# Kernel optimization log

Hardware: AMD Instinct MI355X
Metric: run time of the kernel (lower is better)

Reference implementation:

```python
import jax, jax.numpy as jnp
import numpy as np

B, S, D = 32, 2048, 64

def setup_inputs() -> dict:
    key = jax.random.key(0)
    kq, kk, kv = jax.random.split(key, 3)
    return {
        "query": jax.random.normal(kq, (B, S, D), dtype=jnp.float32),
        "key": jax.random.normal(kk, (B, S, D), dtype=jnp.float32),
        "value": jax.random.normal(kv, (B, S, D), dtype=jnp.float32),
    }

def reference(query, key, value):
    # scores: [B, S, S] = Q @ K^T / sqrt(d_k)  (scale=True)
    d_k = key.shape[-1]
    scores = jnp.einsum("bqd,bkd->bqk", query, key) / jnp.sqrt(jnp.asarray(d_k, query.dtype))
    # exp + normalize over last dim == softmax (no mask, dropout in eval mode)
    attn = jax.nn.softmax(scores, axis=-1)
    # context: [B, S, D] = attn @ V
    context = jnp.einsum("bqk,bkd->bqd", attn, value)
    return context
```

## Files before the change

kernel.cpp:

```cpp
#include <hip/hip_runtime.h>
#include <hip/hip_bf16.h>

#define B_   32
#define S_   2048
#define D_   64
#define KVB  64
#define NT   (S_/KVB)
#define NW   8
#define QW   32
#define QB   (NW*QW)

typedef __attribute__((ext_vector_type(8)))  __bf16 bf16x8;
typedef __attribute__((ext_vector_type(4)))  __bf16 bf16x4;
typedef __attribute__((ext_vector_type(16))) float  f32x16;

__device__ __forceinline__ float fexp2(float x) {
#if __has_builtin(__builtin_amdgcn_exp2f)
    return __builtin_amdgcn_exp2f(x);
#else
    return exp2f(x);
#endif
}

__device__ __forceinline__ unsigned pk2(float a, float b) {
    unsigned r;
    asm("v_cvt_pk_bf16_f32 %0, %1, %2" : "=v"(r) : "v"(a), "v"(b));
    return r;
}

__device__ __forceinline__ void pl32swap(unsigned &a, unsigned &b) {
#if __has_builtin(__builtin_amdgcn_permlane32_swap)
    auto r = __builtin_amdgcn_permlane32_swap(a, b, false, false);
    a = (unsigned)r[0]; b = (unsigned)r[1];
#else
    unsigned pa = (unsigned)__shfl_xor((int)a, 32);
    unsigned pb = (unsigned)__shfl_xor((int)b, 32);
    bool hi = (threadIdx.x & 32) != 0;
    unsigned na = hi ? pb : a;
    unsigned nb = hi ? b  : pa;
    a = na; b = nb;
#endif
}

__device__ __forceinline__ f32x16 z16() {
    f32x16 z;
    #pragma unroll
    for (int i = 0; i < 16; ++i) z[i] = 0.f;
    return z;
}

struct PBpair { bf16x8 a, b; };

__device__ __forceinline__ PBpair pack2(const f32x16 ps) {
    unsigned y0 = pk2(ps[0],  ps[1]);
    unsigned y1 = pk2(ps[2],  ps[3]);
    unsigned y2 = pk2(ps[4],  ps[5]);
    unsigned y3 = pk2(ps[6],  ps[7]);
    pl32swap(y0, y2); pl32swap(y1, y3);
    unsigned z0 = pk2(ps[8],  ps[9]);
    unsigned z1 = pk2(ps[10], ps[11]);
    unsigned z2 = pk2(ps[12], ps[13]);
    unsigned z3 = pk2(ps[14], ps[15]);
    pl32swap(z0, z2); pl32swap(z1, z3);
    union { unsigned u[4]; bf16x8 v; } pa, pbu;
    pa.u[0]=y0;  pa.u[1]=y1;  pa.u[2]=y2;  pa.u[3]=y3;
    pbu.u[0]=z0; pbu.u[1]=z1; pbu.u[2]=z2; pbu.u[3]=z3;
    PBpair r; r.a = pa.v; r.b = pbu.v; return r;
}

__global__ __launch_bounds__(512, 2)
void attn_fwd(const float* __restrict__ Q, const float* __restrict__ K,
              const float* __restrict__ V, float* __restrict__ Out)
{
    __shared__ __align__(16) __bf16 Kt[2][KVB * D_];
    __shared__ __align__(16) __bf16 Vt[2][D_ * KVB];

    const int tid  = threadIdx.x;
    const int w    = tid >> 6;
    const int lane = tid & 63;
    const int l31  = lane & 31;
    const int hi   = lane >> 5;

    const int bid = blockIdx.x;
    const int swz = ((bid & 7) << 5) | (bid >> 3);
    const int b   = swz >> 3;
    const int q0  = (swz & 7) * QB;

    const float SCL = 0.18033688011112042f;
    const float* qp = Q + ((size_t)(b*S_ + q0 + w*QW + l31))*D_ + hi*8;
    bf16x8 qf[4];
    #pragma unroll
    for (int ks = 0; ks < 4; ++ks) {
        float4 f0 = *reinterpret_cast<const float4*>(qp + ks*16);
        float4 f1 = *reinterpret_cast<const float4*>(qp + ks*16 + 4);
        bf16x8 a;
        a[0]=(__bf16)(f0.x*SCL); a[1]=(__bf16)(f0.y*SCL);
        a[2]=(__bf16)(f0.z*SCL); a[3]=(__bf16)(f0.w*SCL);
        a[4]=(__bf16)(f1.x*SCL); a[5]=(__bf16)(f1.y*SCL);
        a[6]=(__bf16)(f1.z*SCL); a[7]=(__bf16)(f1.w*SCL);
        qf[ks]=a;
    }

    const int swzk = (l31 & 7) << 4;
    int offK[4];
    #pragma unroll
    for (int i = 0; i < 4; ++i)
        offK[i] = l31*128 + (((i*32) + hi*16) ^ swzk);

    const float* kg = K + (size_t)b*S_*D_;
    const float* vg = V + (size_t)b*S_*D_;

    const int krow0 = tid >> 4;
    const int kcol  = (tid & 15) * 4;
    const int kwr0  = krow0*128 + ((kcol*2) ^ ((krow0 & 7) << 4));
    const int kwr1  = kwr0 + 32*128;

    const int kv0 = (tid >> 4) * 2;
    const int db  = (tid & 15) * 2;
    int vwr[4];
    #pragma unroll
    for (int j = 0; j < 4; ++j) {
        int d = db + (j >> 1)*32 + (j & 1);
        vwr[j] = d*128 + ((kv0*2) ^ ((d & 7) << 4));
    }

    {
        float4 ka  = *reinterpret_cast<const float4*>(kg + krow0*64 + kcol);
        float4 kb  = *reinterpret_cast<const float4*>(kg + (krow0+32)*64 + kcol);
        float2 va0 = *reinterpret_cast<const float2*>(vg + kv0*64 + db);
        float2 vb0 = *reinterpret_cast<const float2*>(vg + (kv0+1)*64 + db);
        float2 va1 = *reinterpret_cast<const float2*>(vg + kv0*64 + db + 32);
        float2 vb1 = *reinterpret_cast<const float2*>(vg + (kv0+1)*64 + db + 32);
        char* kw = (char*)&Kt[0][0];
        char* vw = (char*)&Vt[0][0];
        bf16x4 h0 = {(__bf16)ka.x,(__bf16)ka.y,(__bf16)ka.z,(__bf16)ka.w};
        bf16x4 h1 = {(__bf16)kb.x,(__bf16)kb.y,(__bf16)kb.z,(__bf16)kb.w};
        *reinterpret_cast<bf16x4*>(kw + kwr0) = h0;
        *reinterpret_cast<bf16x4*>(kw + kwr1) = h1;
        *reinterpret_cast<unsigned*>(vw + vwr[0]) = pk2(va0.x, vb0.x);
        *reinterpret_cast<unsigned*>(vw + vwr[1]) = pk2(va0.y, vb0.y);
        *reinterpret_cast<unsigned*>(vw + vwr[2]) = pk2(va1.x, vb1.x);
        *reinterpret_cast<unsigned*>(vw + vwr[3]) = pk2(va1.y, vb1.y);
    }
    __syncthreads();

    float m_ = -INFINITY, l_ = 0.f;
    f32x16 o0 = z16(), o1 = z16();

    #pragma unroll 2
    for (int t = 0; t < NT; ++t) {
        const int cur = t & 1;

        const int tn = (t+1 < NT) ? (t+1) : t;
        const float* kt_ = kg + tn*KVB*D_;
        const float* vt_ = vg + tn*KVB*D_;
        float4 ka  = *reinterpret_cast<const float4*>(kt_ + krow0*64 + kcol);
        float4 kb  = *reinterpret_cast<const float4*>(kt_ + (krow0+32)*64 + kcol);
        float2 va0 = *reinterpret_cast<const float2*>(vt_ + kv0*64 + db);
        float2 vb0 = *reinterpret_cast<const float2*>(vt_ + (kv0+1)*64 + db);
        float2 va1 = *reinterpret_cast<const float2*>(vt_ + kv0*64 + db + 32);
        float2 vb1 = *reinterpret_cast<const float2*>(vt_ + (kv0+1)*64 + db + 32);

        const char* kbuf = (const char*)&Kt[cur][0];
        const char* vbuf = (const char*)&Vt[cur][0];

        f32x16 s0 = z16(), s1 = z16();
        __builtin_amdgcn_s_setprio(1);
        #pragma unroll
        for (int ks = 0; ks < 4; ++ks) {
            bf16x8 k0 = *reinterpret_cast<const bf16x8*>(kbuf + offK[ks]);
            bf16x8 k1 = *reinterpret_cast<const bf16x8*>(kbuf + offK[ks] + 4096);
            s0 = __builtin_amdgcn_mfma_f32_32x32x16_bf16(k0, qf[ks], s0, 0,0,0);
            s1 = __builtin_amdgcn_mfma_f32_32x32x16_bf16(k1, qf[ks], s1, 0,0,0);
        }
        __builtin_amdgcn_s_setprio(0);

        float pmax = s0[0];
        #pragma unroll
        for (int r = 1; r < 16; ++r) pmax = fmaxf(pmax, s0[r]);
        #pragma unroll
        for (int r = 0; r < 16; ++r) pmax = fmaxf(pmax, s1[r]);
        pmax = fmaxf(pmax, __shfl_xor(pmax, 32));
        if (!__all(pmax - m_ <= 8.0f)) {
            float mn  = fmaxf(m_, pmax);
            float fac = fexp2(m_ - mn);
            m_ = mn; l_ *= fac;
            #pragma unroll
            for (int r = 0; r < 16; ++r) { o0[r] *= fac; o1[r] *= fac; }
        }
        float lsum = 0.f;
        #pragma unroll
        for (int r = 0; r < 16; ++r) { s0[r] = fexp2(s0[r] - m_); lsum += s0[r]; }
        #pragma unroll
        for (int r = 0; r < 16; ++r) { s1[r] = fexp2(s1[r] - m_); lsum += s1[r]; }
        lsum += __shfl_xor(lsum, 32);
        l_ += lsum;

        PBpair p01 = pack2(s0);
        PBpair p23 = pack2(s1);

        __builtin_amdgcn_s_setprio(1);
        #define PV_STEP(c, pbf)                                                        \
        {   bf16x8 v0 = *reinterpret_cast<const bf16x8*>(vbuf + offK[c]);              \
            bf16x8 v1 = *reinterpret_cast<const bf16x8*>(vbuf + offK[c] + 4096);       \
            o0 = __builtin_amdgcn_mfma_f32_32x32x16_bf16(v0, pbf, o0, 0,0,0);          \
            o1 = __builtin_amdgcn_mfma_f32_32x32x16_bf16(v1, pbf, o1, 0,0,0);          }
        PV_STEP(0, p01.a)
        PV_STEP(1, p01.b)
        PV_STEP(2, p23.a)
        PV_STEP(3, p23.b)
        #undef PV_STEP
        __builtin_amdgcn_s_setprio(0);

        if (t+1 < NT) {
            char* kw = (char*)&Kt[cur^1][0];
            char* vw = (char*)&Vt[cur^1][0];
            bf16x4 h0 = {(__bf16)ka.x,(__bf16)ka.y,(__bf16)ka.z,(__bf16)ka.w};
            bf16x4 h1 = {(__bf16)kb.x,(__bf16)kb.y,(__bf16)kb.z,(__bf16)kb.w};
            *reinterpret_cast<bf16x4*>(kw + kwr0) = h0;
            *reinterpret_cast<bf16x4*>(kw + kwr1) = h1;
            *reinterpret_cast<unsigned*>(vw + vwr[0]) = pk2(va0.x, vb0.x);
            *reinterpret_cast<unsigned*>(vw + vwr[1]) = pk2(va0.y, vb0.y);
            *reinterpret_cast<unsigned*>(vw + vwr[2]) = pk2(va1.x, vb1.x);
            *reinterpret_cast<unsigned*>(vw + vwr[3]) = pk2(va1.y, vb1.y);
        }
        __syncthreads();
    }

    float invl = 1.0f / l_;
    float* orow = Out + ((size_t)(b*S_ + q0 + w*QW + l31))*D_;
    #pragma unroll
    for (int rr = 0; rr < 4; ++rr) {
        float4 res;
        res.x = o0[rr*4+0]*invl; res.y = o0[rr*4+1]*invl;
        res.z = o0[rr*4+2]*invl; res.w = o0[rr*4+3]*invl;
        *reinterpret_cast<float4*>(orow + rr*8 + hi*4) = res;
    }
    #pragma unroll
    for (int rr = 0; rr < 4; ++rr) {
        float4 res;
        res.x = o1[rr*4+0]*invl; res.y = o1[rr*4+1]*invl;
        res.z = o1[rr*4+2]*invl; res.w = o1[rr*4+3]*invl;
        *reinterpret_cast<float4*>(orow + 32 + rr*8 + hi*4) = res;
    }
}

extern "C" void kernel_launch(void* const* d_in, const int* in_sizes, int n_in,
                              void* d_out, int out_size, void* d_ws, size_t ws_size,
                              hipStream_t stream) {
    const float* Q = (const float*)d_in[0];
    const float* K = (const float*)d_in[1];
    const float* V = (const float*)d_in[2];
    float* O = (float*)d_out;
    attn_fwd<<<dim3(B_ * (S_ / QB)), dim3(512), 0, stream>>>(Q, K, V, O);
}
```

Before: 56.49 us.

## Halve workgroup to four waves and turn softmax reductions into trees

Cuts each workgroup from 8 to 4 waves (128 query rows), so the grid doubles to 512 blocks. The block swizzle is updated, and each thread now stages twice as many K/V elements per tile into LDS. The row max and row sum are also rewritten as pairwise tree reductions to shorten the serial dependency chains. The aim is better load balance across CUs and more latency hiding, at the cost of each K/V tile being loaded and converted by twice as many blocks and more registers per thread.

After: 66.34 us. +17.4%, slower.

```diff
diff --git a/kernel.cpp b/kernel.cpp
--- a/kernel.cpp
+++ b/kernel.cpp
@@ -6,7 +6,7 @@
 #define D_   64
 #define KVB  64
 #define NT   (S_/KVB)
-#define NW   8
+#define NW   4
 #define QW   32
 #define QB   (NW*QW)
 
@@ -68,7 +68,7 @@
     PBpair r; r.a = pa.v; r.b = pbu.v; return r;
 }
 
-__global__ __launch_bounds__(512, 2)
+__global__ __launch_bounds__(256, 2)
 void attn_fwd(const float* __restrict__ Q, const float* __restrict__ K,
               const float* __restrict__ V, float* __restrict__ Out)
 {
@@ -82,9 +82,9 @@
     const int hi   = lane >> 5;
 
     const int bid = blockIdx.x;
-    const int swz = ((bid & 7) << 5) | (bid >> 3);
-    const int b   = swz >> 3;
-    const int q0  = (swz & 7) * QB;
+    const int swz = ((bid & 7) << 6) | (bid >> 3);
+    const int b   = swz >> 4;
+    const int q0  = (swz & 15) * QB;
 
     const float SCL = 0.18033688011112042f;
     const float* qp = Q + ((size_t)(b*S_ + q0 + w*QW + l31))*D_ + hi*8;
@@ -113,34 +113,34 @@
     const int krow0 = tid >> 4;
     const int kcol  = (tid & 15) * 4;
     const int kwr0  = krow0*128 + ((kcol*2) ^ ((krow0 & 7) << 4));
-    const int kwr1  = kwr0 + 32*128;
 
     const int kv0 = (tid >> 4) * 2;
     const int db  = (tid & 15) * 2;
-    int vwr[4];
-    #pragma unroll
-    for (int j = 0; j < 4; ++j) {
-        int d = db + (j >> 1)*32 + (j & 1);
-        vwr[j] = d*128 + ((kv0*2) ^ ((d & 7) << 4));
-    }
+    const int vwr0 = db*128     + ((kv0*2) ^ ((db & 7) << 4));
+    const int vwr1 = (db+1)*128 + ((kv0*2) ^ (((db+1) & 7) << 4));
 
     {
-        float4 ka  = *reinterpret_cast<const float4*>(kg + krow0*64 + kcol);
-        float4 kb  = *reinterpret_cast<const float4*>(kg + (krow0+32)*64 + kcol);
-        float2 va0 = *reinterpret_cast<const float2*>(vg + kv0*64 + db);
-        float2 vb0 = *reinterpret_cast<const float2*>(vg + (kv0+1)*64 + db);
-        float2 va1 = *reinterpret_cast<const float2*>(vg + kv0*64 + db + 32);
-        float2 vb1 = *reinterpret_cast<const float2*>(vg + (kv0+1)*64 + db + 32);
         char* kw = (char*)&Kt[0][0];
         char* vw = (char*)&Vt[0][0];
-        bf16x4 h0 = {(__bf16)ka.x,(__bf16)ka.y,(__bf16)ka.z,(__bf16)ka.w};
-        bf16x4 h1 = {(__bf16)kb.x,(__bf16)kb.y,(__bf16)kb.z,(__bf16)kb.w};
-        *reinterpret_cast<bf16x4*>(kw + kwr0) = h0;
-        *reinterpret_cast<bf16x4*>(kw + kwr1) = h1;
-        *reinterpret_cast<unsigned*>(vw + vwr[0]) = pk2(va0.x, vb0.x);
-        *reinterpret_cast<unsigned*>(vw + vwr[1]) = pk2(va0.y, vb0.y);
-        *reinterpret_cast<unsigned*>(vw + vwr[2]) = pk2(va1.x, vb1.x);
-        *reinterpret_cast<unsigned*>(vw + vwr[3]) = pk2(va1.y, vb1.y);
+        #pragma unroll
+        for (int j = 0; j < 4; ++j) {
+            float4 f = *reinterpret_cast<const float4*>(kg + (krow0 + 16*j)*64 + kcol);
+            bf16x4 h = {(__bf16)f.x,(__bf16)f.y,(__bf16)f.z,(__bf16)f.w};
+            *reinterpret_cast<bf16x4*>(kw + kwr0 + j*2048) = h;
+        }
+        #pragma unroll
+        for (int half = 0; half < 2; ++half) {
+            int kvr = kv0 + half*32;
+            int x   = half ? 64 : 0;
+            float2 r0a = *reinterpret_cast<const float2*>(vg + kvr*64 + db);
+            float2 r1a = *reinterpret_cast<const float2*>(vg + (kvr+1)*64 + db);
+            float2 r0b = *reinterpret_cast<const float2*>(vg + kvr*64 + db + 32);
+            float2 r1b = *reinterpret_cast<const float2*>(vg + (kvr+1)*64 + db + 32);
+            *reinterpret_cast<unsigned*>(vw + (vwr0 ^ x))        = pk2(r0a.x, r1a.x);
+            *reinterpret_cast<unsigned*>(vw + (vwr1 ^ x))        = pk2(r0a.y, r1a.y);
+            *reinterpret_cast<unsigned*>(vw + (vwr0 ^ x) + 4096) = pk2(r0b.x, r1b.x);
+            *reinterpret_cast<unsigned*>(vw + (vwr1 ^ x) + 4096) = pk2(r0b.y, r1b.y);
+        }
     }
     __syncthreads();
 
@@ -154,12 +154,18 @@
         const int tn = (t+1 < NT) ? (t+1) : t;
         const float* kt_ = kg + tn*KVB*D_;
         const float* vt_ = vg + tn*KVB*D_;
-        float4 ka  = *reinterpret_cast<const float4*>(kt_ + krow0*64 + kcol);
-        float4 kb  = *reinterpret_cast<const float4*>(kt_ + (krow0+32)*64 + kcol);
-        float2 va0 = *reinterpret_cast<const float2*>(vt_ + kv0*64 + db);
-        float2 vb0 = *reinterpret_cast<const float2*>(vt_ + (kv0+1)*64 + db);
-        float2 va1 = *reinterpret_cast<const float2*>(vt_ + kv0*64 + db + 32);
-        float2 vb1 = *reinterpret_cast<const float2*>(vt_ + (kv0+1)*64 + db + 32);
+        float4 ka0 = *reinterpret_cast<const float4*>(kt_ + krow0*64 + kcol);
+        float4 ka1 = *reinterpret_cast<const float4*>(kt_ + (krow0+16)*64 + kcol);
+        float4 ka2 = *reinterpret_cast<const float4*>(kt_ + (krow0+32)*64 + kcol);
+        float4 ka3 = *reinterpret_cast<const float4*>(kt_ + (krow0+48)*64 + kcol);
+        float2 v0a = *reinterpret_cast<const float2*>(vt_ + kv0*64 + db);
+        float2 v1a = *reinterpret_cast<const float2*>(vt_ + (kv0+1)*64 + db);
+        float2 v0b = *reinterpret_cast<const float2*>(vt_ + kv0*64 + db + 32);
+        float2 v1b = *reinterpret_cast<const float2*>(vt_ + (kv0+1)*64 + db + 32);
+        float2 v2a = *reinterpret_cast<const float2*>(vt_ + (kv0+32)*64 + db);
+        float2 v3a = *reinterpret_cast<const float2*>(vt_ + (kv0+33)*64 + db);
+        float2 v2b = *reinterpret_cast<const float2*>(vt_ + (kv0+32)*64 + db + 32);
+        float2 v3b = *reinterpret_cast<const float2*>(vt_ + (kv0+33)*64 + db + 32);
 
         const char* kbuf = (const char*)&Kt[cur][0];
         const char* vbuf = (const char*)&Vt[cur][0];
@@ -175,12 +181,14 @@
         }
         __builtin_amdgcn_s_setprio(0);
 
-        float pmax = s0[0];
-        #pragma unroll
-        for (int r = 1; r < 16; ++r) pmax = fmaxf(pmax, s0[r]);
-        #pragma unroll
-        for (int r = 0; r < 16; ++r) pmax = fmaxf(pmax, s1[r]);
-        pmax = fmaxf(pmax, __shfl_xor(pmax, 32));
+        float tmx[16];
+        #pragma unroll
+        for (int i = 0; i < 16; ++i) tmx[i] = fmaxf(s0[i], s1[i]);
+        #pragma unroll
+        for (int st = 8; st > 0; st >>= 1)
+            #pragma unroll
+            for (int i = 0; i < st; ++i) tmx[i] = fmaxf(tmx[i], tmx[i+st]);
+        float pmax = fmaxf(tmx[0], __shfl_xor(tmx[0], 32));
         if (!__all(pmax - m_ <= 8.0f)) {
             float mn  = fmaxf(m_, pmax);
             float fac = fexp2(m_ - mn);
@@ -188,13 +196,18 @@
             #pragma unroll
             for (int r = 0; r < 16; ++r) { o0[r] *= fac; o1[r] *= fac; }
         }
-        float lsum = 0.f;
-        #pragma unroll
-        for (int r = 0; r < 16; ++r) { s0[r] = fexp2(s0[r] - m_); lsum += s0[r]; }
-        #pragma unroll
-        for (int r = 0; r < 16; ++r) { s1[r] = fexp2(s1[r] - m_); lsum += s1[r]; }
-        lsum += __shfl_xor(lsum, 32);
-        l_ += lsum;
+        #pragma unroll
+        for (int r = 0; r < 16; ++r) s0[r] = fexp2(s0[r] - m_);
+        #pragma unroll
+        for (int r = 0; r < 16; ++r) s1[r] = fexp2(s1[r] - m_);
+        float tsm[16];
+        #pragma unroll
+        for (int i = 0; i < 16; ++i) tsm[i] = s0[i] + s1[i];
+        #pragma unroll
+        for (int st = 8; st > 0; st >>= 1)
+            #pragma unroll
+            for (int i = 0; i < st; ++i) tsm[i] += tsm[i+st];
+        l_ += tsm[0] + __shfl_xor(tsm[0], 32);
 
         PBpair p01 = pack2(s0);
         PBpair p23 = pack2(s1);
@@ -215,14 +228,22 @@
         if (t+1 < NT) {
             char* kw = (char*)&Kt[cur^1][0];
             char* vw = (char*)&Vt[cur^1][0];
-            bf16x4 h0 = {(__bf16)ka.x,(__bf16)ka.y,(__bf16)ka.z,(__bf16)ka.w};
-            bf16x4 h1 = {(__bf16)kb.x,(__bf16)kb.y,(__bf16)kb.z,(__bf16)kb.w};
-            *reinterpret_cast<bf16x4*>(kw + kwr0) = h0;
-            *reinterpret_cast<bf16x4*>(kw + kwr1) = h1;
-            *reinterpret_cast<unsigned*>(vw + vwr[0]) = pk2(va0.x, vb0.x);
-            *reinterpret_cast<unsigned*>(vw + vwr[1]) = pk2(va0.y, vb0.y);
-            *reinterpret_cast<unsigned*>(vw + vwr[2]) = pk2(va1.x, vb1.x);
-            *reinterpret_cast<unsigned*>(vw + vwr[3]) = pk2(va1.y, vb1.y);
+            bf16x4 h0 = {(__bf16)ka0.x,(__bf16)ka0.y,(__bf16)ka0.z,(__bf16)ka0.w};
+            bf16x4 h1 = {(__bf16)ka1.x,(__bf16)ka1.y,(__bf16)ka1.z,(__bf16)ka1.w};
+            bf16x4 h2 = {(__bf16)ka2.x,(__bf16)ka2.y,(__bf16)ka2.z,(__bf16)ka2.w};
+            bf16x4 h3 = {(__bf16)ka3.x,(__bf16)ka3.y,(__bf16)ka3.z,(__bf16)ka3.w};
+            *reinterpret_cast<bf16x4*>(kw + kwr0)        = h0;
+            *reinterpret_cast<bf16x4*>(kw + kwr0 + 2048) = h1;
+            *reinterpret_cast<bf16x4*>(kw + kwr0 + 4096) = h2;
+            *reinterpret_cast<bf16x4*>(kw + kwr0 + 6144) = h3;
+            *reinterpret_cast<unsigned*>(vw + vwr0)        = pk2(v0a.x, v1a.x);
+            *reinterpret_cast<unsigned*>(vw + vwr1)        = pk2(v0a.y, v1a.y);
+            *reinterpret_cast<unsigned*>(vw + vwr0 + 4096) = pk2(v0b.x, v1b.x);
+            *reinterpret_cast<unsigned*>(vw + vwr1 + 4096) = pk2(v0b.y, v1b.y);
+            *reinterpret_cast<unsigned*>(vw + (vwr0 ^ 64))        = pk2(v2a.x, v3a.x);
+            *reinterpret_cast<unsigned*>(vw + (vwr1 ^ 64))        = pk2(v2a.y, v3a.y);
+            *reinterpret_cast<unsigned*>(vw + (vwr0 ^ 64) + 4096) = pk2(v2b.x, v3b.x);
+            *reinterpret_cast<unsigned*>(vw + (vwr1 ^ 64) + 4096) = pk2(v2b.y, v3b.y);
         }
         __syncthreads();
     }
@@ -252,5 +273,5 @@
     const float* K = (const float*)d_in[1];
     const float* V = (const float*)d_in[2];
     float* O = (float*)d_out;
-    attn_fwd<<<dim3(B_ * (S_ / QB)), dim3(512), 0, stream>>>(Q, K, V, O);
-}
+    attn_fwd<<<dim3(B_ * (S_ / QB)), dim3(256), 0, stream>>>(Q, K, V, O);
+}
```
